# Optimization experiments

Measured on AMD Instinct MI355X. Metric: run time of the kernel, lower is better.

Reference implementation:

```python
import jax, jax.numpy as jnp
import numpy as np


def setup_inputs() -> dict:
    key = jax.random.key(0)
    k1, k2, k3, k4 = jax.random.split(key, 4)
    B, N, F = 16, 2048, 512
    return {
        "source": jax.random.normal(k1, (B, N, 3), dtype=jnp.float32),
        "target": jax.random.normal(k2, (B, N, 3), dtype=jnp.float32),
        "fsource": jax.random.normal(k3, (B, F, N), dtype=jnp.float32),
        "ftarget": jax.random.normal(k4, (B, F, N), dtype=jnp.float32),
    }


def reference(source, target, fsource, ftarget):
    # source/target: (B, N, 3) -> (B, 3, N)
    src = jnp.swapaxes(source, 1, 2)
    tgt = jnp.swapaxes(target, 1, 2)

    # soft correspondence: logits[b, i, j] = <ftarget[b,:,i], fsource[b,:,j]>
    logits = jnp.einsum('bfi,bfj->bij', ftarget, fsource)  # (B, Nt, Ns)
    weight = jax.nn.softmax(logits, axis=1)  # softmax over target points (dim=1)

    # predicted target for each source point: (B, 3, Ns)
    pred_tgt = jnp.einsum('bci,bij->bcj', tgt, weight)

    src_mean = jnp.mean(src, axis=2, keepdims=True)        # (B, 3, 1)
    tgt_mean = jnp.mean(pred_tgt, axis=2, keepdims=True)   # (B, 3, 1)
    src_res = src - src_mean
    tgt_res = pred_tgt - tgt_mean

    # 3x3 cross-covariance per batch item
    S = jnp.einsum('bcn,bdn->bcd', src_res, tgt_res)  # (B, 3, 3)

    # torch.svd: S = U diag(Sig) V^T ; jnp.linalg.svd: S = U diag(Sig) Vh
    U, Sig, Vh = jnp.linalg.svd(S, full_matrices=False)
    V = jnp.swapaxes(Vh, 1, 2)
    UT = jnp.swapaxes(U, 1, 2)

    d = jnp.linalg.det(jnp.matmul(V, UT))  # (B,)
    B = S.shape[0]
    M = jnp.tile(jnp.eye(3, dtype=S.dtype)[None], (B, 1, 1))
    M = M.at[:, 2, 2].set(d)

    Rot = jnp.matmul(jnp.matmul(V, M), UT)                     # (B, 3, 3)
    tr = (tgt_mean - jnp.matmul(Rot, src_mean))[..., 0]        # (B, 3)
    return (Rot, tr)
```

## Files before the change

kernel.cpp:

```cpp
#include <hip/hip_runtime.h>
#include <math.h>
#include <stdint.h>

#define NB   16
#define NPT  2048
#define NF   512
#define BI   128
#define BJ   128
#define KB   32
#define NTHR 512
#define NJT  (NPT / BJ)
#define NIT  (NPT / BI)
#define NKC  (NF / KB)
#define NIQ  4

#define CGB1     1024
#define KCSLAB1  (128 * CGB1)
#define TPB1     ((size_t)NB * NKC * KCSLAB1)

#define CGS    1056
#define PLANE  8448
#define PLANE_H 4224
#define BPLANE 16896
#define BUF2   50688

typedef _Float16 h4 __attribute__((ext_vector_type(4)));
typedef _Float16 h8 __attribute__((ext_vector_type(8)));
typedef float    f32x4 __attribute__((ext_vector_type(4)));

#define TRR(dst, a) asm volatile("ds_read_b64_tr_b16 %0, %1" : "=v"(dst) : "v"(a))

#define MF(A, B, C) __builtin_amdgcn_mfma_f32_16x16x32_f16(A, B, C, 0, 0, 0)

__device__ __forceinline__ void gld16(const void* g, void* l) {
    __builtin_amdgcn_global_load_lds(
        (const __attribute__((address_space(1))) unsigned int*)g,
        (__attribute__((address_space(3))) unsigned int*)l, 16, 0, 0);
}

__device__ __forceinline__ h8 cat(h4 a, h4 b) {
    return __builtin_shufflevector(a, b, 0, 1, 2, 3, 4, 5, 6, 7);
}

__device__ __forceinline__ void cvt8(const float4 a, const float4 b, h8& hi, h8& lo) {
    hi[0] = (_Float16)a.x; hi[1] = (_Float16)a.y;
    hi[2] = (_Float16)a.z; hi[3] = (_Float16)a.w;
    hi[4] = (_Float16)b.x; hi[5] = (_Float16)b.y;
    hi[6] = (_Float16)b.z; hi[7] = (_Float16)b.w;
    lo[0] = (_Float16)(a.x - (float)hi[0]);
    lo[1] = (_Float16)(a.y - (float)hi[1]);
    lo[2] = (_Float16)(a.z - (float)hi[2]);
    lo[3] = (_Float16)(a.w - (float)hi[3]);
    lo[4] = (_Float16)(b.x - (float)hi[4]);
    lo[5] = (_Float16)(b.y - (float)hi[5]);
    lo[6] = (_Float16)(b.z - (float)hi[6]);
    lo[7] = (_Float16)(b.w - (float)hi[7]);
}

__device__ __forceinline__ h8 cvt8h(const float4 a, const float4 b) {
    h8 hi;
    hi[0] = (_Float16)a.x; hi[1] = (_Float16)a.y;
    hi[2] = (_Float16)a.z; hi[3] = (_Float16)a.w;
    hi[4] = (_Float16)b.x; hi[5] = (_Float16)b.y;
    hi[6] = (_Float16)b.z; hi[7] = (_Float16)b.w;
    return hi;
}

__device__ __forceinline__ int hoffB(int f, int n8) {
    return (n8 >> 1) * CGS + (f >> 4) * 512 + ((f >> 2) & 3) * 128
         + (f & 3) * 32 + (n8 & 1) * 16;
}

__global__ __launch_bounds__(256)
void prepass_kernel(const float* __restrict__ fsource,
                    const float* __restrict__ ftarget,
                    _Float16* __restrict__ tiled)
{
    const int b  = blockIdx.x;
    const int kc = blockIdx.y;
    const int z  = blockIdx.z;
    const int tensor = z >> 3;
    const int cgrp   = z & 7;
    const float* src = (tensor == 0 ? ftarget : fsource)
                     + (size_t)b * NF * NPT + (size_t)kc * KB * NPT + cgrp * 256;
    char* dst = (char*)tiled + (size_t)tensor * TPB1
              + ((size_t)(b * NKC + kc) * 128 + cgrp * 16) * CGB1;

    __shared__ _Float16 sm[8448];
    const int t   = threadIdx.x;
    const int kk8 = t >> 5;
    const int c8  = (t & 31) * 8;
    const int cg  = c8 >> 4;
    const int cl  = c8 & 15;

    #pragma unroll
    for (int rep = 0; rep < 4; ++rep) {
        const int k = rep * 8 + kk8;
        const float4 v0 = *(const float4*)(src + (size_t)k * NPT + c8);
        const float4 v1 = *(const float4*)(src + (size_t)k * NPT + c8 + 4);
        const h8 hi = cvt8h(v0, v1);
        const int kh = k >> 4, kr = k & 15, kg = kr >> 2, j = kr & 3;
        *(h8*)((char*)sm + cg * 1056 + kh * 512 + kg * 128 + j * 32 + cl * 2) = hi;
    }
    __syncthreads();
    #pragma unroll
    for (int q = 0; q < 4; ++q) {
        const int off = q * 4096 + t * 16;
        const int ocg = off >> 10, rem = off & 1023;
        *(float4*)(dst + off) = *(const float4*)((char*)sm + ocg * 1056 + rem);
    }
}

__global__ __launch_bounds__(256, 2)
void attn_state_tiled(const float* __restrict__ target,
                      const _Float16* __restrict__ tiled,
                      float* __restrict__ stw)
{
    const int b    = blockIdx.x;
    const int jt   = blockIdx.y;
    const int iq   = blockIdx.z;
    const int j0   = jt * BJ;
    const int tid  = threadIdx.x;
    const int lane = tid & 63;
    const int wave = tid >> 6;
    const int wi   = wave >> 1;
    const int wj   = wave & 1;
    const int lg   = lane >> 4;
    const int lr   = lane & 15;

    __shared__ __align__(16) char TIL[3][16384];
    __shared__ float  tgtsAll[3][512];
    __shared__ float  redM[2][BJ];
    __shared__ float4 redS[2][BJ];

    const uint32_t tilesBase = (uint32_t)(uintptr_t)&TIL[0][0];
    const uint32_t trLane    = (uint32_t)(lane * 8);

    const char* Atile = (const char*)tiled;
    const char* Btile = (const char*)tiled + TPB1;

    {
        const float* tg = target + ((size_t)b * NPT + iq * 512) * 3;
        #pragma unroll
        for (int k = 0; k < 6; ++k) {
            const int p = tid + k * 256;
            tgtsAll[p % 3][p / 3] = tg[p];
        }
    }
    __syncthreads();

    float Mrun[4], Zrun[4], Yrun[4][3];
    #pragma unroll
    for (int n = 0; n < 4; ++n) {
        Mrun[n] = -3.0e38f; Zrun[n] = 0.0f;
        Yrun[n][0] = 0.0f; Yrun[n][1] = 0.0f; Yrun[n][2] = 0.0f;
    }

#define STAGE1(kcv, dstbuf) { \
    const size_t slab = (size_t)(b * NKC + (kcv)) * KCSLAB1; \
    const size_t ao = slab + (size_t)(i0 >> 4) * CGB1 + lane * 16; \
    const size_t bo = slab + (size_t)(j0 >> 4) * CGB1 + lane * 16; \
    char* lb = &TIL[dstbuf][0]; \
    gld16(Atile + ao + wave * 1024,       lb + wave * 1024); \
    gld16(Atile + ao + (wave + 4) * 1024, lb + (wave + 4) * 1024); \
    gld16(Btile + bo + wave * 1024,       lb + 8192 + wave * 1024); \
    gld16(Btile + bo + (wave + 4) * 1024, lb + 8192 + (wave + 4) * 1024); }

#define RD_A1(m) TRR(ta[m][0], aB + (m) * CGB1); \
                 TRR(ta[m][1], aB + (m) * CGB1 + 512);
#define RD_B1(n) TRR(tb[n][0], bB + (n) * CGB1); \
                 TRR(tb[n][1], bB + (n) * CGB1 + 512);
#define WAITK(N) asm volatile("s_waitcnt lgkmcnt(" #N ")" ::: "memory"); \
                 __builtin_amdgcn_sched_barrier(0);
#define MROW1(M) \
    { const h8 Ah = cat(ta[M][0], ta[M][1]); \
      acc[M][0] = MF(Ah, Bh[0], acc[M][0]); \
      acc[M][1] = MF(Ah, Bh[1], acc[M][1]); \
      acc[M][2] = MF(Ah, Bh[2], acc[M][2]); \
      acc[M][3] = MF(Ah, Bh[3], acc[M][3]); }

    for (int it = 0; it < 4; ++it) {
        const int i0 = iq * 512 + it * BI;

        STAGE1(0, 0)
        STAGE1(1, 1)
        asm volatile("s_waitcnt vmcnt(4)" ::: "memory");
        __builtin_amdgcn_sched_barrier(0);
        __syncthreads();

        f32x4 acc[4][4];
        #pragma unroll
        for (int m = 0; m < 4; ++m)
            #pragma unroll
            for (int n = 0; n < 4; ++n)
                acc[m][n] = (f32x4){0.0f, 0.0f, 0.0f, 0.0f};

        for (int kc = 0; kc < NKC; ++kc) {
            const int buf = kc % 3;
            if (kc + 2 < NKC) STAGE1(kc + 2, (kc + 2) % 3)

            const uint32_t aB = tilesBase + (uint32_t)buf * 16384
                              + (uint32_t)(wi * 4) * CGB1 + trLane;
            const uint32_t bB = tilesBase + (uint32_t)buf * 16384 + 8192u
                              + (uint32_t)(wj * 4) * CGB1 + trLane;
            h4 ta[4][2], tb[4][2];
            h8 Bh[4];

            __builtin_amdgcn_s_setprio(1);
            RD_A1(0) RD_B1(0) RD_B1(1) RD_B1(2) RD_B1(3)
            RD_A1(1) RD_A1(2) RD_A1(3)
            WAITK(6)
            Bh[0] = cat(tb[0][0], tb[0][1]);
            Bh[1] = cat(tb[1][0], tb[1][1]);
            Bh[2] = cat(tb[2][0], tb[2][1]);
            Bh[3] = cat(tb[3][0], tb[3][1]);
            MROW1(0)
            WAITK(4) MROW1(1)
            WAITK(2) MROW1(2)
            WAITK(0) MROW1(3)
            __builtin_amdgcn_s_setprio(0);

            if (kc + 2 < NKC) {
                asm volatile("s_waitcnt vmcnt(4)" ::: "memory");
            } else {
                asm volatile("s_waitcnt vmcnt(0)" ::: "memory");
            }
            __builtin_amdgcn_sched_barrier(0);
            __syncthreads();
        }

        #pragma unroll
        for (int n = 0; n < 4; ++n) {
            float m = acc[0][n][0];
            #pragma unroll
            for (int mm = 0; mm < 4; ++mm)
                #pragma unroll
                for (int r = 0; r < 4; ++r)
                    m = fmaxf(m, acc[mm][n][r]);
            m = fmaxf(m, __shfl_xor(m, 16));
            m = fmaxf(m, __shfl_xor(m, 32));
            if (lane < 16) redM[wi][wj * 64 + n * 16 + lr] = m;
        }
        __syncthreads();
        float mnew[4];
        #pragma unroll
        for (int n = 0; n < 4; ++n) {
            const int col = wj * 64 + n * 16 + lr;
            mnew[n] = fmaxf(Mrun[n], fmaxf(redM[0][col], redM[1][col]));
        }

        float z[4] = {0, 0, 0, 0}, y[4][3] = {{0,0,0},{0,0,0},{0,0,0},{0,0,0}};
        #pragma unroll
        for (int mm = 0; mm < 4; ++mm)
            #pragma unroll
            for (int r = 0; r < 4; ++r) {
                const int iL = it * BI + wi * 64 + mm * 16 + lg * 4 + r;
                const float t0 = tgtsAll[0][iL], t1 = tgtsAll[1][iL], t2 = tgtsAll[2][iL];
                #pragma unroll
                for (int n = 0; n < 4; ++n) {
                    const float e = __expf(acc[mm][n][r] - mnew[n]);
                    z[n] += e;
                    y[n][0] = fmaf(e, t0, y[n][0]);
                    y[n][1] = fmaf(e, t1, y[n][1]);
                    y[n][2] = fmaf(e, t2, y[n][2]);
                }
            }
        #pragma unroll
        for (int n = 0; n < 4; ++n) {
            #pragma unroll
            for (int off = 16; off <= 32; off <<= 1) {
                z[n]    += __shfl_xor(z[n], off);
                y[n][0] += __shfl_xor(y[n][0], off);
                y[n][1] += __shfl_xor(y[n][1], off);
                y[n][2] += __shfl_xor(y[n][2], off);
            }
            if (lane < 16)
                redS[wi][wj * 64 + n * 16 + lr] = make_float4(z[n], y[n][0], y[n][1], y[n][2]);
        }
        __syncthreads();
        #pragma unroll
        for (int n = 0; n < 4; ++n) {
            const int col = wj * 64 + n * 16 + lr;
            const float4 s0 = redS[0][col], s1 = redS[1][col];
            const float sc = __expf(Mrun[n] - mnew[n]);
            Zrun[n]    = Zrun[n]    * sc + s0.x + s1.x;
            Yrun[n][0] = Yrun[n][0] * sc + s0.y + s1.y;
            Yrun[n][1] = Yrun[n][1] * sc + s0.z + s1.z;
            Yrun[n][2] = Yrun[n][2] * sc + s0.w + s1.w;
            Mrun[n] = mnew[n];
        }
        __syncthreads();
    }

    if (wi == 0 && lane < 16) {
        const int SP4 = NB * NIQ * NPT;
        #pragma unroll
        for (int n = 0; n < 4; ++n) {
            const int j   = j0 + wj * 64 + n * 16 + lr;
            const int idx = (b * NIQ + iq) * NPT + j;
            stw[idx]           = Mrun[n];
            stw[SP4 + idx]     = Zrun[n];
            stw[2 * SP4 + idx] = Yrun[n][0];
            stw[3 * SP4 + idx] = Yrun[n][1];
            stw[4 * SP4 + idx] = Yrun[n][2];
        }
    }
#undef STAGE1
#undef RD_A1
#undef RD_B1
#undef WAITK
#undef MROW1
}

__global__ void combine4_kernel(const float* __restrict__ source,
                                const float* __restrict__ stw,
                                float* __restrict__ partials)
{
    const int b   = blockIdx.x;
    const int jc  = blockIdx.y;
    const int tid = threadIdx.x;
    const int lane = tid & 63, wv = tid >> 6;
    const int j = jc * BJ + tid;
    const int SP = NB * NIQ * NPT;

    __shared__ float fin2[2][15];

    float m[NIQ], zz[NIQ], yy0[NIQ], yy1[NIQ], yy2[NIQ];
    #pragma unroll
    for (int q = 0; q < NIQ; ++q) {
        const int idx = (b * NIQ + q) * NPT + j;
        m[q]   = stw[idx];
        zz[q]  = stw[SP + idx];
        yy0[q] = stw[2 * SP + idx];
        yy1[q] = stw[3 * SP + idx];
        yy2[q] = stw[4 * SP + idx];
    }
    float ms = m[0];
    #pragma unroll
    for (int q = 1; q < NIQ; ++q) ms = fmaxf(ms, m[q]);
    float Z = 0, Y0 = 0, Y1 = 0, Y2 = 0;
    #pragma unroll
    for (int q = 0; q < NIQ; ++q) {
        const float s = __expf(m[q] - ms);
        Z  += zz[q]  * s;
        Y0 += yy0[q] * s;
        Y1 += yy1[q] * s;
        Y2 += yy2[q] * s;
    }
    const float iz = 1.0f / Z;
    const float p0 = Y0 * iz, p1 = Y1 * iz, p2 = Y2 * iz;

    const float* sp = source + ((size_t)b * NPT + j) * 3;
    const float s0 = sp[0], s1 = sp[1], s2 = sp[2];

    float v[15];
    v[0] = s0; v[1] = s1; v[2] = s2;
    v[3] = p0; v[4] = p1; v[5] = p2;
    v[6]  = s0 * p0; v[7]  = s0 * p1; v[8]  = s0 * p2;
    v[9]  = s1 * p0; v[10] = s1 * p1; v[11] = s1 * p2;
    v[12] = s2 * p0; v[13] = s2 * p1; v[14] = s2 * p2;

    #pragma unroll
    for (int q = 0; q < 15; ++q)
        #pragma unroll
        for (int off = 32; off > 0; off >>= 1)
            v[q] += __shfl_down(v[q], off);
    if (lane == 0) {
        #pragma unroll
        for (int q = 0; q < 15; ++q) fin2[wv][q] = v[q];
    }
    __syncthreads();
    if (tid == 0) {
        float* o = partials + (((size_t)b << 4) + jc) * 16;
        #pragma unroll
        for (int q = 0; q < 15; ++q) o[q] = fin2[0][q] + fin2[1][q];
    }
}

__global__ void combine_kernel(const float* __restrict__ source,
                               const float* __restrict__ stw,
                               float* __restrict__ partials)
{
    const int b   = blockIdx.x;
    const int jc  = blockIdx.y;
    const int tid = threadIdx.x;
    const int lane = tid & 63, wv = tid >> 6;
    const int j = jc * BJ + tid;
    const int SP = NB * 2 * NPT;
    const int i0 = (b * 2 + 0) * NPT + j;
    const int i1 = (b * 2 + 1) * NPT + j;

    __shared__ float fin2[2][15];

    const float ma = stw[i0],      mb = stw[i1];
    const float za = stw[SP + i0], zb = stw[SP + i1];
    const float ms = fmaxf(ma, mb);
    const float sa = __expf(ma - ms), sb = __expf(mb - ms);
    const float zt = za * sa + zb * sb;
    const float iz = 1.0f / zt;
    const float p0 = (stw[2 * SP + i0] * sa + stw[2 * SP + i1] * sb) * iz;
    const float p1 = (stw[3 * SP + i0] * sa + stw[3 * SP + i1] * sb) * iz;
    const float p2 = (stw[4 * SP + i0] * sa + stw[4 * SP + i1] * sb) * iz;

    const float* sp = source + ((size_t)b * NPT + j) * 3;
    const float s0 = sp[0], s1 = sp[1], s2 = sp[2];

    float v[15];
    v[0] = s0; v[1] = s1; v[2] = s2;
    v[3] = p0; v[4] = p1; v[5] = p2;
    v[6]  = s0 * p0; v[7]  = s0 * p1; v[8]  = s0 * p2;
    v[9]  = s1 * p0; v[10] = s1 * p1; v[11] = s1 * p2;
    v[12] = s2 * p0; v[13] = s2 * p1; v[14] = s2 * p2;

    #pragma unroll
    for (int q = 0; q < 15; ++q)
        #pragma unroll
        for (int off = 32; off > 0; off >>= 1)
            v[q] += __shfl_down(v[q], off);
    if (lane == 0) {
        #pragma unroll
        for (int q = 0; q < 15; ++q) fin2[wv][q] = v[q];
    }
    __syncthreads();
    if (tid == 0) {
        float* o = partials + (((size_t)b << 4) + jc) * 16;
        #pragma unroll
        for (int q = 0; q < 15; ++q) o[q] = fin2[0][q] + fin2[1][q];
    }
}

__global__ __launch_bounds__(NTHR, 2)
void attn_state_kernel(const float* __restrict__ target,
                       const float* __restrict__ fsource,
                       const float* __restrict__ ftarget,
                       float* __restrict__ stw)
{
    const int b    = blockIdx.x;
    const int jt   = blockIdx.y;
    const int ih   = blockIdx.z;
    const int j0   = jt * 256;
    const int tid  = threadIdx.x;
    const int lane = tid & 63;
    const int wave = tid >> 6;
    const int wi   = wave >> 2;
    const int wj   = wave & 3;
    const int lg   = lane >> 4;
    const int lr   = lane & 15;

    __shared__ __align__(16) unsigned char TIL[2][BUF2];
    __shared__ float  tgts[3][BI];
    __shared__ float  redM[2][256];
    __shared__ float4 redS[2][256];

    const uint32_t tilesBase = (uint32_t)(uintptr_t)&TIL[0][0];
    const uint32_t trLane    = (uint32_t)(lane * 8);
    const size_t   fbase     = (size_t)b * NF * NPT;

    const int fA  = tid >> 4,  n8A  = tid & 15;
    const int fB0 = tid >> 5,  n8B  = tid & 31;
    const int fB1 = (tid + 512) >> 5;
    const int offA  = hoffB(fA, n8A);
    const int offB0 = hoffB(fB0, n8B);
    const int offB1 = hoffB(fB1, n8B);

    float Mrun[4], Zrun[4], Yrun[4][3];
    #pragma unroll
    for (int n = 0; n < 4; ++n) {
        Mrun[n] = -3.0e38f; Zrun[n] = 0.0f;
        Yrun[n][0] = 0.0f; Yrun[n][1] = 0.0f; Yrun[n][2] = 0.0f;
    }

#define RD_B(n) TRR(tb[n][0][0], bB + (n) * CGS); \
                TRR(tb[n][0][1], bB + (n) * CGS + 512); \
                TRR(tb[n][1][0], bB + (n) * CGS + BPLANE); \
                TRR(tb[n][1][1], bB + (n) * CGS + BPLANE + 512);
#define RD_A(m) TRR(ta[m][0][0], aB + (m) * CGS); \
                TRR(ta[m][0][1], aB + (m) * CGS + 512); \
                TRR(ta[m][1][0], aB + (m) * CGS + PLANE); \
                TRR(ta[m][1][1], aB + (m) * CGS + PLANE + 512);
#define BBLD(n) Bh[n] = cat(tb[n][0][0], tb[n][0][1]); \
                Bl[n] = cat(tb[n][1][0], tb[n][1][1]);
#define MM3(M, N) \
    acc[M][N] = MF(Ah, Bh[N], acc[M][N]); \
    acc[M][N] = MF(Ah, Bl[N], acc[M][N]); \
    acc[M][N] = MF(Al, Bh[N], acc[M][N]);
#define MSTEP(M, WAITSTR) \
    asm volatile("s_waitcnt lgkmcnt(" WAITSTR ")" ::: "memory"); \
    __builtin_amdgcn_sched_barrier(0); \
    { const h8 Ah = cat(ta[M][0][0], ta[M][0][1]); \
      const h8 Al = cat(ta[M][1][0], ta[M][1][1]); \
      MM3(M, 0) MM3(M, 1) MM3(M, 2) MM3(M, 3) }

    for (int it = 0; it < 8; ++it) {
        const int i0 = ih * 1024 + it * BI;

        const float* pA  = ftarget + fbase + (size_t)fA  * NPT + i0 + n8A * 8;
        const float* pB0 = fsource + fbase + (size_t)fB0 * NPT + j0 + n8B * 8;
        const float* pB1 = fsource + fbase + (size_t)fB1 * NPT + j0 + n8B * 8;

        {
            float4 a0  = *(const float4*)(pA);
            float4 a1  = *(const float4*)(pA + 4);
            float4 b00 = *(const float4*)(pB0);
            float4 b01 = *(const float4*)(pB0 + 4);
            float4 b10 = *(const float4*)(pB1);
            float4 b11 = *(const float4*)(pB1 + 4);
            if (tid < BI) {
                const float* tp = target + ((size_t)b * NPT + i0 + tid) * 3;
                tgts[0][tid] = tp[0]; tgts[1][tid] = tp[1]; tgts[2][tid] = tp[2];
            }
            unsigned char* bp = (unsigned char*)&TIL[0][0];
            h8 hi, lo;
            cvt8(a0, a1, hi, lo);
            *(h8*)(bp + offA) = hi;  *(h8*)(bp + PLANE + offA) = lo;
            cvt8(b00, b01, hi, lo);
            *(h8*)(bp + 2 * PLANE + offB0) = hi;  *(h8*)(bp + 2 * PLANE + BPLANE + offB0) = lo;
            cvt8(b10, b11, hi, lo);
            *(h8*)(bp + 2 * PLANE + offB1) = hi;  *(h8*)(bp + 2 * PLANE + BPLANE + offB1) = lo;
        }
        __syncthreads();

        f32x4 acc[4][4];
        #pragma unroll
        for (int m = 0; m < 4; ++m)
            #pragma unroll
            for (int n = 0; n < 4; ++n)
                acc[m][n] = (f32x4){0.0f, 0.0f, 0.0f, 0.0f};

        for (int kc = 0; kc < NKC; ++kc) {
            const int buf = kc & 1;
            float4 ga0, ga1, gb00, gb01, gb10, gb11;
            if (kc + 1 < NKC) {
                const size_t ko = (size_t)(kc + 1) * KB * NPT;
                ga0  = *(const float4*)(pA + ko);
                ga1  = *(const float4*)(pA + ko + 4);
                gb00 = *(const float4*)(pB0 + ko);
                gb01 = *(const float4*)(pB0 + ko + 4);
                gb10 = *(const float4*)(pB1 + ko);
                gb11 = *(const float4*)(pB1 + ko + 4);
            }

            const uint32_t bb = tilesBase + (uint32_t)buf * BUF2;
            const uint32_t aB = bb + (uint32_t)(wi * 4) * CGS + trLane;
            const uint32_t bB = bb + 2u * PLANE + (uint32_t)(wj * 4) * CGS + trLane;
            h4 ta[4][2][2], tb[4][2][2];
            h8 Bh[4], Bl[4];

            __builtin_amdgcn_s_setprio(1);
            RD_B(0) RD_B(1) RD_B(2) RD_B(3)
            RD_A(0) RD_A(1) RD_A(2) RD_A(3)
            asm volatile("s_waitcnt lgkmcnt(12)" ::: "memory");
            __builtin_amdgcn_sched_barrier(0);
            BBLD(0) BBLD(1) BBLD(2) BBLD(3)
            {
                const h8 Ah = cat(ta[0][0][0], ta[0][0][1]);
                const h8 Al = cat(ta[0][1][0], ta[0][1][1]);
                MM3(0, 0) MM3(0, 1) MM3(0, 2) MM3(0, 3)
            }
            MSTEP(1, "8")
            MSTEP(2, "4")
            MSTEP(3, "0")
            __builtin_amdgcn_s_setprio(0);

            if (kc + 1 < NKC) {
                unsigned char* bp = (unsigned char*)&TIL[0][0] + (buf ^ 1) * BUF2;
                h8 hi, lo;
                cvt8(ga0, ga1, hi, lo);
                *(h8*)(bp + offA) = hi;  *(h8*)(bp + PLANE + offA) = lo;
                cvt8(gb00, gb01, hi, lo);
                *(h8*)(bp + 2 * PLANE + offB0) = hi;  *(h8*)(bp + 2 * PLANE + BPLANE + offB0) = lo;
                cvt8(gb10, gb11, hi, lo);
                *(h8*)(bp + 2 * PLANE + offB1) = hi;  *(h8*)(bp + 2 * PLANE + BPLANE + offB1) = lo;
                __syncthreads();
            }
        }

        #pragma unroll
        for (int n = 0; n < 4; ++n) {
            float m = acc[0][n][0];
            #pragma unroll
            for (int mm = 0; mm < 4; ++mm)
                #pragma unroll
                for (int r = 0; r < 4; ++r)
                    m = fmaxf(m, acc[mm][n][r]);
            m = fmaxf(m, __shfl_xor(m, 16));
            m = fmaxf(m, __shfl_xor(m, 32));
            if (lane < 16) redM[wi][wj * 64 + n * 16 + lr] = m;
        }
        __syncthreads();
        float mnew[4];
        #pragma unroll
        for (int n = 0; n < 4; ++n) {
            const int col = wj * 64 + n * 16 + lr;
            mnew[n] = fmaxf(Mrun[n], fmaxf(redM[0][col], redM[1][col]));
        }

        float z[4] = {0, 0, 0, 0}, y[4][3] = {{0,0,0},{0,0,0},{0,0,0},{0,0,0}};
        #pragma unroll
        for (int mm = 0; mm < 4; ++mm)
            #pragma unroll
            for (int r = 0; r < 4; ++r) {
                const int iL = wi * 64 + mm * 16 + lg * 4 + r;
                const float t0 = tgts[0][iL], t1 = tgts[1][iL], t2 = tgts[2][iL];
                #pragma unroll
                for (int n = 0; n < 4; ++n) {
                    const float e = __expf(acc[mm][n][r] - mnew[n]);
                    z[n] += e;
                    y[n][0] = fmaf(e, t0, y[n][0]);
                    y[n][1] = fmaf(e, t1, y[n][1]);
                    y[n][2] = fmaf(e, t2, y[n][2]);
                }
            }
        #pragma unroll
        for (int n = 0; n < 4; ++n) {
            #pragma unroll
            for (int off = 16; off <= 32; off <<= 1) {
                z[n]    += __shfl_xor(z[n], off);
                y[n][0] += __shfl_xor(y[n][0], off);
                y[n][1] += __shfl_xor(y[n][1], off);
                y[n][2] += __shfl_xor(y[n][2], off);
            }
            if (lane < 16)
                redS[wi][wj * 64 + n * 16 + lr] = make_float4(z[n], y[n][0], y[n][1], y[n][2]);
        }
        __syncthreads();
        #pragma unroll
        for (int n = 0; n < 4; ++n) {
            const int col = wj * 64 + n * 16 + lr;
            const float4 s0 = redS[0][col], s1 = redS[1][col];
            const float sc = __expf(Mrun[n] - mnew[n]);
            Zrun[n]    = Zrun[n]    * sc + s0.x + s1.x;
            Yrun[n][0] = Yrun[n][0] * sc + s0.y + s1.y;
            Yrun[n][1] = Yrun[n][1] * sc + s0.z + s1.z;
            Yrun[n][2] = Yrun[n][2] * sc + s0.w + s1.w;
            Mrun[n] = mnew[n];
        }
        __syncthreads();
    }

    if (wi == 0 && lane < 16) {
        #pragma unroll
        for (int n = 0; n < 4; ++n) {
            const int j   = j0 + wj * 64 + n * 16 + lr;
            const int idx = (b * 2 + ih) * NPT + j;
            stw[0 * (NB * 2 * NPT) + idx] = Mrun[n];
            stw[1 * (NB * 2 * NPT) + idx] = Zrun[n];
            stw[2 * (NB * 2 * NPT) + idx] = Yrun[n][0];
            stw[3 * (NB * 2 * NPT) + idx] = Yrun[n][1];
            stw[4 * (NB * 2 * NPT) + idx] = Yrun[n][2];
        }
    }
#undef RD_B
#undef RD_A
#undef BBLD
#undef MM3
#undef MSTEP
}

__device__ inline void jrot(float A[3][3], float V[3][3], int p, int q)
{
    const float apq = A[p][q];
    if (fabsf(apq) < 1e-28f) return;
    const float tau = (A[q][q] - A[p][p]) / (2.0f * apq);
    const float t   = (tau >= 0.0f ? 1.0f : -1.0f) / (fabsf(tau) + sqrtf(1.0f + tau * tau));
    const float c   = rsqrtf(1.0f + t * t);
    const float s   = t * c;
    const float app = A[p][p], aqq = A[q][q];
    A[p][p] = app - t * apq;
    A[q][q] = aqq + t * apq;
    A[p][q] = 0.0f; A[q][p] = 0.0f;
    const int r = 3 - p - q;
    const float arp = A[r][p], arq = A[r][q];
    A[r][p] = c * arp - s * arq; A[p][r] = A[r][p];
    A[r][q] = s * arp + c * arq; A[q][r] = A[r][q];
    #pragma unroll
    for (int rr = 0; rr < 3; ++rr) {
        const float vrp = V[rr][p], vrq = V[rr][q];
        V[rr][p] = c * vrp - s * vrq;
        V[rr][q] = s * vrp + c * vrq;
    }
}

__global__ void svd_finalize_kernel(const float* __restrict__ partials,
                                    float* __restrict__ out)
{
    const int b = threadIdx.x;
    if (b >= NB) return;

    float srcS[3] = {0, 0, 0}, predS[3] = {0, 0, 0}, SP[9] = {0, 0, 0, 0, 0, 0, 0, 0, 0};
    for (int p = 0; p < NJT; ++p) {
        const float* vv = partials + (((size_t)b << 4) + p) * 16;
        srcS[0] += vv[0]; srcS[1] += vv[1]; srcS[2] += vv[2];
        predS[0] += vv[3]; predS[1] += vv[4]; predS[2] += vv[5];
        #pragma unroll
        for (int q = 0; q < 9; ++q) SP[q] += vv[6 + q];
    }

    const float invN = 1.0f / (float)NPT;
    float ms[3], mt[3];
    #pragma unroll
    for (int c = 0; c < 3; ++c) { ms[c] = srcS[c] * invN; mt[c] = predS[c] * invN; }

    float S[3][3];
    #pragma unroll
    for (int c = 0; c < 3; ++c)
        #pragma unroll
        for (int d = 0; d < 3; ++d)
            S[c][d] = SP[c * 3 + d] - srcS[c] * predS[d] * invN;

    float A[3][3];
    #pragma unroll
    for (int i = 0; i < 3; ++i)
        #pragma unroll
        for (int j = 0; j < 3; ++j)
            A[i][j] = S[0][i] * S[0][j] + S[1][i] * S[1][j] + S[2][i] * S[2][j];

    float V[3][3] = {{1, 0, 0}, {0, 1, 0}, {0, 0, 1}};
    for (int sweep = 0; sweep < 12; ++sweep) {
        jrot(A, V, 0, 1);
        jrot(A, V, 0, 2);
        jrot(A, V, 1, 2);
    }

    float lam[3] = {A[0][0], A[1][1], A[2][2]};
    for (int i = 0; i < 2; ++i) {
        int mx = i;
        for (int j = i + 1; j < 3; ++j) if (lam[j] > lam[mx]) mx = j;
        if (mx != i) {
            const float tl = lam[i]; lam[i] = lam[mx]; lam[mx] = tl;
            #pragma unroll
            for (int r = 0; r < 3; ++r) {
                const float tv = V[r][i]; V[r][i] = V[r][mx]; V[r][mx] = tv;
            }
        }
    }

    float w0[3], w1[3], u1[3], u2[3], u3[3];
    #pragma unroll
    for (int r = 0; r < 3; ++r) {
        w0[r] = S[r][0] * V[0][0] + S[r][1] * V[1][0] + S[r][2] * V[2][0];
        w1[r] = S[r][0] * V[0][1] + S[r][1] * V[1][1] + S[r][2] * V[2][1];
    }
    const float n1 = sqrtf(w0[0] * w0[0] + w0[1] * w0[1] + w0[2] * w0[2]) + 1e-30f;
    #pragma unroll
    for (int r = 0; r < 3; ++r) u1[r] = w0[r] / n1;
    const float d01 = u1[0] * w1[0] + u1[1] * w1[1] + u1[2] * w1[2];
    #pragma unroll
    for (int r = 0; r < 3; ++r) u2[r] = w1[r] - d01 * u1[r];
    const float n2 = sqrtf(u2[0] * u2[0] + u2[1] * u2[1] + u2[2] * u2[2]) + 1e-30f;
    #pragma unroll
    for (int r = 0; r < 3; ++r) u2[r] /= n2;
    u3[0] = u1[1] * u2[2] - u1[2] * u2[1];
    u3[1] = u1[2] * u2[0] - u1[0] * u2[2];
    u3[2] = u1[0] * u2[1] - u1[1] * u2[0];

    const float detV =
        V[0][0] * (V[1][1] * V[2][2] - V[1][2] * V[2][1]) -
        V[0][1] * (V[1][0] * V[2][2] - V[1][2] * V[2][0]) +
        V[0][2] * (V[1][0] * V[2][1] - V[1][1] * V[2][0]);

    float R[3][3];
    #pragma unroll
    for (int r = 0; r < 3; ++r)
        #pragma unroll
        for (int c = 0; c < 3; ++c)
            R[r][c] = V[r][0] * u1[c] + V[r][1] * u2[c] + detV * V[r][2] * u3[c];

    #pragma unroll
    for (int r = 0; r < 3; ++r)
        #pragma unroll
        for (int c = 0; c < 3; ++c)
            out[b * 9 + r * 3 + c] = R[r][c];

    #pragma unroll
    for (int r = 0; r < 3; ++r) {
        const float tr = mt[r] - (R[r][0] * ms[0] + R[r][1] * ms[1] + R[r][2] * ms[2]);
        out[NB * 9 + b * 3 + r] = tr;
    }
}

extern "C" void kernel_launch(void* const* d_in, const int* in_sizes, int n_in,
                              void* d_out, int out_size, void* d_ws, size_t ws_size,
                              hipStream_t stream)
{
    const float* source  = (const float*)d_in[0];
    const float* target  = (const float*)d_in[1];
    const float* fsource = (const float*)d_in[2];
    const float* ftarget = (const float*)d_in[3];
    float* out = (float*)d_out;

    const size_t PART_FLOATS = (size_t)NB * 16 * 16;
    const size_t ST4_FLOATS  = (size_t)5 * NB * NIQ * NPT;
    const size_t ST2_FLOATS  = (size_t)5 * NB * 2 * NPT;
    const size_t NEED_BIG    = 2 * TPB1 + (ST4_FLOATS + PART_FLOATS) * 4;

    if (ws_size >= NEED_BIG) {
        _Float16* tiled = (_Float16*)d_ws;
        float* stw      = (float*)((char*)d_ws + 2 * TPB1);
        float* partials = stw + ST4_FLOATS;
        prepass_kernel<<<dim3(NB, NKC, 16), 256, 0, stream>>>(fsource, ftarget, tiled);
        attn_state_tiled<<<dim3(NB, 16, NIQ), 256, 0, stream>>>(target, tiled, stw);
        combine4_kernel<<<dim3(NB, 16), 128, 0, stream>>>(source, stw, partials);
        svd_finalize_kernel<<<1, 64, 0, stream>>>(partials, out);
    } else {
        float* stw      = (float*)d_ws;
        float* partials = stw + ST2_FLOATS;
        attn_state_kernel<<<dim3(NB, 8, 2), NTHR, 0, stream>>>(target, fsource, ftarget, stw);
        combine_kernel<<<dim3(NB, 16), 128, 0, stream>>>(source, stw, partials);
        svd_finalize_kernel<<<1, 64, 0, stream>>>(partials, out);
    }
}
```

Baseline: 144.3 us.

## Switch GEMM k-loop to double-buffered 64-wide K stages with fewer barriers

Replaces the triple-buffered 32-wide K pipeline (prefetch distance two) with a double-buffered scheme where each stage loads two K slabs (64 wide) into a 32 KB buffer. Each stage now runs two MFMA half-steps before one barrier, so the loop takes half as many __syncthreads calls. In exchange, prefetch lookahead is only one stage and the wait drains all outstanding loads (vmcnt(0)) every iteration. LDS for the tiles grows from 48 KB to 64 KB, which may hurt occupancy at 2 blocks per CU.

```diff
diff --git a/kernel.cpp b/kernel.cpp
--- a/kernel.cpp
+++ b/kernel.cpp
@@ -128,7 +128,7 @@
     const int lg   = lane >> 4;
     const int lr   = lane & 15;
 
-    __shared__ __align__(16) char TIL[3][16384];
+    __shared__ __align__(16) char TIL[2][32768];
     __shared__ float  tgtsAll[3][512];
     __shared__ float  redM[2][BJ];
     __shared__ float4 redS[2][BJ];
@@ -156,15 +156,20 @@
         Yrun[n][0] = 0.0f; Yrun[n][1] = 0.0f; Yrun[n][2] = 0.0f;
     }
 
-#define STAGE1(kcv, dstbuf) { \
-    const size_t slab = (size_t)(b * NKC + (kcv)) * KCSLAB1; \
-    const size_t ao = slab + (size_t)(i0 >> 4) * CGB1 + lane * 16; \
-    const size_t bo = slab + (size_t)(j0 >> 4) * CGB1 + lane * 16; \
+#define STAGE2(kc2v, dstbuf) { \
+    const size_t slab0 = (size_t)(b * NKC + 2 * (kc2v)) * KCSLAB1; \
+    const size_t slab1 = slab0 + KCSLAB1; \
+    const size_t aoff  = (size_t)(i0 >> 4) * CGB1 + lane * 16; \
+    const size_t boff  = (size_t)(j0 >> 4) * CGB1 + lane * 16; \
     char* lb = &TIL[dstbuf][0]; \
-    gld16(Atile + ao + wave * 1024,       lb + wave * 1024); \
-    gld16(Atile + ao + (wave + 4) * 1024, lb + (wave + 4) * 1024); \
-    gld16(Btile + bo + wave * 1024,       lb + 8192 + wave * 1024); \
-    gld16(Btile + bo + (wave + 4) * 1024, lb + 8192 + (wave + 4) * 1024); }
+    gld16(Atile + slab0 + aoff + wave * 1024,       lb + wave * 1024); \
+    gld16(Atile + slab0 + aoff + (wave + 4) * 1024, lb + (wave + 4) * 1024); \
+    gld16(Atile + slab1 + aoff + wave * 1024,       lb + 8192 + wave * 1024); \
+    gld16(Atile + slab1 + aoff + (wave + 4) * 1024, lb + 8192 + (wave + 4) * 1024); \
+    gld16(Btile + slab0 + boff + wave * 1024,       lb + 16384 + wave * 1024); \
+    gld16(Btile + slab0 + boff + (wave + 4) * 1024, lb + 16384 + (wave + 4) * 1024); \
+    gld16(Btile + slab1 + boff + wave * 1024,       lb + 24576 + wave * 1024); \
+    gld16(Btile + slab1 + boff + (wave + 4) * 1024, lb + 24576 + (wave + 4) * 1024); }
 
 #define RD_A1(m) TRR(ta[m][0], aB + (m) * CGB1); \
                  TRR(ta[m][1], aB + (m) * CGB1 + 512);
@@ -179,12 +184,28 @@
       acc[M][2] = MF(Ah, Bh[2], acc[M][2]); \
       acc[M][3] = MF(Ah, Bh[3], acc[M][3]); }
 
+#define KHALF(hofs) { \
+    const uint32_t aB = bufB + (hofs) + (uint32_t)(wi * 4) * CGB1 + trLane; \
+    const uint32_t bB = bufB + 16384u + (hofs) + (uint32_t)(wj * 4) * CGB1 + trLane; \
+    h4 ta[4][2], tb[4][2]; \
+    h8 Bh[4]; \
+    RD_A1(0) RD_B1(0) RD_B1(1) RD_B1(2) RD_B1(3) \
+    RD_A1(1) RD_A1(2) RD_A1(3) \
+    WAITK(6) \
+    Bh[0] = cat(tb[0][0], tb[0][1]); \
+    Bh[1] = cat(tb[1][0], tb[1][1]); \
+    Bh[2] = cat(tb[2][0], tb[2][1]); \
+    Bh[3] = cat(tb[3][0], tb[3][1]); \
+    MROW1(0) \
+    WAITK(4) MROW1(1) \
+    WAITK(2) MROW1(2) \
+    WAITK(0) MROW1(3) }
+
     for (int it = 0; it < 4; ++it) {
         const int i0 = iq * 512 + it * BI;
 
-        STAGE1(0, 0)
-        STAGE1(1, 1)
-        asm volatile("s_waitcnt vmcnt(4)" ::: "memory");
+        STAGE2(0, 0)
+        asm volatile("s_waitcnt vmcnt(0)" ::: "memory");
         __builtin_amdgcn_sched_barrier(0);
         __syncthreads();
 
@@ -195,36 +216,17 @@
             for (int n = 0; n < 4; ++n)
                 acc[m][n] = (f32x4){0.0f, 0.0f, 0.0f, 0.0f};
 
-        for (int kc = 0; kc < NKC; ++kc) {
-            const int buf = kc % 3;
-            if (kc + 2 < NKC) STAGE1(kc + 2, (kc + 2) % 3)
-
-            const uint32_t aB = tilesBase + (uint32_t)buf * 16384
-                              + (uint32_t)(wi * 4) * CGB1 + trLane;
-            const uint32_t bB = tilesBase + (uint32_t)buf * 16384 + 8192u
-                              + (uint32_t)(wj * 4) * CGB1 + trLane;
-            h4 ta[4][2], tb[4][2];
-            h8 Bh[4];
-
+        for (int kc2 = 0; kc2 < 8; ++kc2) {
+            const int buf = kc2 & 1;
+            if (kc2 + 1 < 8) STAGE2(kc2 + 1, buf ^ 1)
+
+            const uint32_t bufB = tilesBase + (uint32_t)buf * 32768;
             __builtin_amdgcn_s_setprio(1);
-            RD_A1(0) RD_B1(0) RD_B1(1) RD_B1(2) RD_B1(3)
-            RD_A1(1) RD_A1(2) RD_A1(3)
-            WAITK(6)
-            Bh[0] = cat(tb[0][0], tb[0][1]);
-            Bh[1] = cat(tb[1][0], tb[1][1]);
-            Bh[2] = cat(tb[2][0], tb[2][1]);
-            Bh[3] = cat(tb[3][0], tb[3][1]);
-            MROW1(0)
-            WAITK(4) MROW1(1)
-            WAITK(2) MROW1(2)
-            WAITK(0) MROW1(3)
+            KHALF(0u)
+            KHALF(8192u)
             __builtin_amdgcn_s_setprio(0);
 
-            if (kc + 2 < NKC) {
-                asm volatile("s_waitcnt vmcnt(4)" ::: "memory");
-            } else {
-                asm volatile("s_waitcnt vmcnt(0)" ::: "memory");
-            }
+            asm volatile("s_waitcnt vmcnt(0)" ::: "memory");
             __builtin_amdgcn_sched_barrier(0);
             __syncthreads();
         }
@@ -305,11 +307,12 @@
             stw[4 * SP4 + idx] = Yrun[n][2];
         }
     }
-#undef STAGE1
+#undef STAGE2
 #undef RD_A1
 #undef RD_B1
 #undef WAITK
 #undef MROW1
+#undef KHALF
 }
 
 __global__ void combine4_kernel(const float* __restrict__ source,
```

After: 144.8 us. Within noise of the previous version (+0.3%).
